# Performance work log

Hardware: AMD Instinct MI355X
Metric: run time of the kernel (lower is better)

## Reference

```python
import jax, jax.numpy as jnp
import numpy as np

N = 20000      # nodes
E = 320000     # edges per metapath graph
M = 3          # metapaths
IN = 256       # input feat dim
HID = 64       # num_hidden per head
NH = 4         # nhead (layer 1)
OUT = 256      # out_dim
NHO = 1        # nhead_out (layer 2)
SA_H = 128     # semantic attention hidden
NEG_SLOPE = 0.2


def gat_conv(h, W, attn_l, attn_r, src, dst, apply_relu):
    # h: [N, F_in]; W: [F_in, H*D]; attn_l/attn_r: [H, D]
    H, D = attn_l.shape
    feat = (h @ W).reshape(N, H, D)                      # [N, H, D]
    el = jnp.sum(feat * attn_l, axis=-1)                 # [N, H]
    er = jnp.sum(feat * attn_r, axis=-1)                 # [N, H]
    e = jax.nn.leaky_relu(el[src] + er[dst], NEG_SLOPE)  # [E, H]
    # edge softmax grouped by destination node
    emax = jax.ops.segment_max(e, dst, num_segments=N)   # [N, H] (-inf for empty)
    emax = jnp.where(jnp.isfinite(emax), emax, 0.0)
    ee = jnp.exp(e - emax[dst])                          # [E, H]
    denom = jax.ops.segment_sum(ee, dst, num_segments=N) # [N, H]
    alpha = ee / (denom[dst] + 1e-9)                     # [E, H]
    msg = alpha[:, :, None] * feat[src]                  # [E, H, D]
    out = jax.ops.segment_sum(msg, dst, num_segments=N)  # [N, H, D]
    out = out.reshape(N, H * D)                          # concat heads
    return jax.nn.relu(out) if apply_relu else out


def semantic_attention(z, W1, b1, v):
    # z: [N, M, F]
    w = jnp.tanh(z @ W1 + b1) @ v          # [N, M, 1]
    w = w.mean(axis=0)                     # [M, 1]
    beta = jax.nn.softmax(w, axis=0)       # [M, 1]
    out = jnp.sum(beta[None, :, :] * z, axis=1)  # [N, F]
    att_mp = beta.squeeze()                # [M]
    return out, att_mp


def setup_inputs() -> dict:
    key = jax.random.key(0)
    ks = jax.random.split(key, 16)
    s = 0.05
    return {
        "x": jax.random.normal(ks[0], (N, IN), dtype=jnp.float32),
        "edges": jax.random.randint(ks[1], (M, 2, E), 0, N, dtype=jnp.int64)
                 if jax.config.jax_enable_x64 else
                 jax.random.randint(ks[1], (M, 2, E), 0, N, dtype=jnp.int32),
        "W1": jax.random.normal(ks[2], (IN, NH * HID), dtype=jnp.float32) * s,
        "al1": jax.random.normal(ks[3], (NH, HID), dtype=jnp.float32) * s,
        "ar1": jax.random.normal(ks[4], (NH, HID), dtype=jnp.float32) * s,
        "saW1": jax.random.normal(ks[5], (NH * HID, SA_H), dtype=jnp.float32) * s,
        "sab1": jnp.zeros((SA_H,), dtype=jnp.float32),
        "sav1": jax.random.normal(ks[6], (SA_H, 1), dtype=jnp.float32) * s,
        "W2": jax.random.normal(ks[7], (NH * HID, NHO * OUT), dtype=jnp.float32) * s,
        "al2": jax.random.normal(ks[8], (NHO, OUT), dtype=jnp.float32) * s,
        "ar2": jax.random.normal(ks[9], (NHO, OUT), dtype=jnp.float32) * s,
        "saW2": jax.random.normal(ks[10], (NHO * OUT, SA_H), dtype=jnp.float32) * s,
        "sab2": jnp.zeros((SA_H,), dtype=jnp.float32),
        "sav2": jax.random.normal(ks[11], (SA_H, 1), dtype=jnp.float32) * s,
    }


def reference(x, edges, W1, al1, ar1, saW1, sab1, sav1,
              W2, al2, ar2, saW2, sab2, sav2):
    h = x
    # HAN layer 1: shared GATConv over each metapath graph, relu activation
    z = jnp.stack([gat_conv(h, W1, al1, ar1, edges[i, 0], edges[i, 1], True)
                   for i in range(M)], axis=1)          # [N, M, NH*HID]
    h, att_mp = semantic_attention(z, saW1, sab1, sav1)
    # HAN layer 2: last layer, no activation (encoding=False)
    z = jnp.stack([gat_conv(h, W2, al2, ar2, edges[i, 0], edges[i, 1], False)
                   for i in range(M)], axis=1)          # [N, M, NHO*OUT]
    h, att_mp = semantic_attention(z, saW2, sab2, sav2)
    return h, att_mp
```

## Files before the change

kernel.cpp:

```cpp
#include <hip/hip_runtime.h>
#include <hip/hip_bf16.h>
#include <math.h>

#define NN 20000
#define EE 320000
#define MM 3
#define FW 256
#define SAH 128
#define NB 79
#define RNG 2500

typedef __attribute__((ext_vector_type(8))) short bf16x8;
typedef __attribute__((ext_vector_type(4))) float f32x4;
typedef __attribute__((ext_vector_type(2))) float f32x2;

static __device__ __forceinline__ float lrelu(float x){ return x > 0.f ? x : 0.2f*x; }

static __device__ __forceinline__ unsigned short f2bf(float f) {
    unsigned u = __float_as_uint(f);
    return (unsigned short)((u + 0x7FFFu + ((u >> 16) & 1u)) >> 16);
}
static __device__ __forceinline__ float bf2f(unsigned short b) {
    return __uint_as_float(((unsigned)b) << 16);
}
static __device__ __forceinline__ float bflo(unsigned u){ return __uint_as_float(u << 16); }
static __device__ __forceinline__ float bfhi(unsigned u){ return __uint_as_float(u & 0xffff0000u); }
static __device__ __forceinline__ unsigned pk2bf(float lo, float hi) {
    return ((unsigned)f2bf(lo)) | (((unsigned)f2bf(hi)) << 16);
}

#define XBLK 2500
#define ZBLK 235
__global__ __launch_bounds__(256) void prep_kernel(const float* __restrict__ x, unsigned short* __restrict__ xb,
                                                   const float* __restrict__ W1, unsigned short* __restrict__ W1t,
                                                   const float* __restrict__ saW1, unsigned short* __restrict__ saW1t,
                                                   const float* __restrict__ W2, unsigned short* __restrict__ W2t,
                                                   const float* __restrict__ saW2, unsigned short* __restrict__ saW2t,
                                                   int* __restrict__ cnt, float* __restrict__ wsum) {
    int b = blockIdx.x, tid = threadIdx.x;
    if (b < XBLK) {
        int i = b*256 + tid;
        const float4* p = (const float4*)x + (size_t)i*2;
        float4 v0 = p[0], v1 = p[1];
        uint4 o;
        o.x = pk2bf(v0.x, v0.y); o.y = pk2bf(v0.z, v0.w);
        o.z = pk2bf(v1.x, v1.y); o.w = pk2bf(v1.z, v1.w);
        ((uint4*)xb)[i] = o;
        return;
    }
    int b2 = b - XBLK;
    if (b2 < 256)      { int n = b2;       W1t  [(size_t)n*256 + tid] = f2bf(W1  [(size_t)tid*256 + n]); return; }
    else if (b2 < 384) { int n = b2 - 256; saW1t[(size_t)n*256 + tid] = f2bf(saW1[(size_t)tid*SAH + n]); return; }
    else if (b2 < 640) { int n = b2 - 384; W2t  [(size_t)n*256 + tid] = f2bf(W2  [(size_t)tid*256 + n]); return; }
    else if (b2 < 768) { int n = b2 - 640; saW2t[(size_t)n*256 + tid] = f2bf(saW2[(size_t)tid*SAH + n]); return; }
    int zb = b2 - 768;
    int i = zb*256 + tid;
    if (i < MM*NN) cnt[i] = 0;
    if (zb == 0 && tid < 8) wsum[tid] = 0.f;
}

__global__ __launch_bounds__(256) void hist_kernel(const int* __restrict__ edges, int* __restrict__ cnt) {
    int m = blockIdx.y;
    int r = blockIdx.x & 7;
    int chunk = blockIdx.x >> 3;
    int e4 = chunk*256 + threadIdx.x;
    if (e4 >= EE/4) return;
    int lo = r * RNG, hi = lo + RNG;
    int4 d = ((const int4*)(edges + (size_t)(m*2+1)*EE))[e4];
    if (d.x >= lo && d.x < hi) atomicAdd(&cnt[m*NN + d.x], 1);
    if (d.y >= lo && d.y < hi) atomicAdd(&cnt[m*NN + d.y], 1);
    if (d.z >= lo && d.z < hi) atomicAdd(&cnt[m*NN + d.z], 1);
    if (d.w >= lo && d.w < hi) atomicAdd(&cnt[m*NN + d.w], 1);
}

__global__ __launch_bounds__(256) void scanA_kernel(const int* __restrict__ cnt, int* __restrict__ rowptr, int* __restrict__ bsum) {
    int m = blockIdx.y;
    int i = blockIdx.x*256 + threadIdx.x;
    int v = (i < NN) ? cnt[m*NN + i] : 0;
    int lane = threadIdx.x & 63;
    int val = v;
    #pragma unroll
    for (int o = 1; o < 64; o <<= 1) { int t = __shfl_up(val, o); if (lane >= o) val += t; }
    __shared__ int ws[4];
    int w = threadIdx.x >> 6;
    if (lane == 63) ws[w] = val;
    __syncthreads();
    #pragma unroll
    for (int j = 0; j < 3; ++j) if (j < w) val += ws[j];
    if (i < NN) rowptr[m*(NN+1) + 1 + i] = val;
    if (threadIdx.x == 255) bsum[m*NB + blockIdx.x] = val;
}

__global__ __launch_bounds__(128) void scanB_kernel(const int* __restrict__ bsum, int* __restrict__ boff) {
    __shared__ int s[128];
    int t = threadIdx.x;
    for (int m = 0; m < MM; ++m) {
        int v = (t < NB) ? bsum[m*NB + t] : 0;
        s[t] = v; __syncthreads();
        for (int o = 1; o < 128; o <<= 1) {
            int x = (t >= o) ? s[t - o] : 0;
            __syncthreads();
            s[t] += x;
            __syncthreads();
        }
        if (t < NB) boff[m*NB + t] = s[t] - v;
        __syncthreads();
    }
}

__global__ __launch_bounds__(256) void scanC_kernel(const int* __restrict__ cnt, int* __restrict__ rowptr,
                                                    const int* __restrict__ boff, int* __restrict__ cursor) {
    int m = blockIdx.y;
    int i = blockIdx.x*256 + threadIdx.x;
    if (i >= NN) return;
    int incl = rowptr[m*(NN+1) + 1 + i] + boff[m*NB + blockIdx.x];
    rowptr[m*(NN+1) + 1 + i] = incl;
    cursor[m*NN + i] = incl - cnt[m*NN + i];
    if (i == 0 && blockIdx.x == 0) rowptr[m*(NN+1)] = 0;
}

__global__ __launch_bounds__(256) void scatter_kernel(const int* __restrict__ edges, int* __restrict__ cursor,
                                                      uint2* __restrict__ csr) {
    int m = blockIdx.y;
    int r = blockIdx.x & 7;
    int chunk = blockIdx.x >> 3;
    int e4 = chunk*256 + threadIdx.x;
    if (e4 >= EE/4) return;
    int lo = r * RNG, hi = lo + RNG;
    int4 s = ((const int4*)(edges + (size_t)(m*2  )*EE))[e4];
    int4 d = ((const int4*)(edges + (size_t)(m*2+1)*EE))[e4];
    if (d.x >= lo && d.x < hi) { int p = atomicAdd(&cursor[m*NN + d.x], 1); csr[(size_t)m*EE + p] = make_uint2((unsigned)s.x, (unsigned)d.x); }
    if (d.y >= lo && d.y < hi) { int p = atomicAdd(&cursor[m*NN + d.y], 1); csr[(size_t)m*EE + p] = make_uint2((unsigned)s.y, (unsigned)d.y); }
    if (d.z >= lo && d.z < hi) { int p = atomicAdd(&cursor[m*NN + d.z], 1); csr[(size_t)m*EE + p] = make_uint2((unsigned)s.z, (unsigned)d.z); }
    if (d.w >= lo && d.w < hi) { int p = atomicAdd(&cursor[m*NN + d.w], 1); csr[(size_t)m*EE + p] = make_uint2((unsigned)s.w, (unsigned)d.w); }
}

template<int H>
__global__ __launch_bounds__(256) void gemm_mfma_kernel(const unsigned short* __restrict__ A,
                                                        const unsigned short* __restrict__ Bt,
                                                        const float* __restrict__ attl, const float* __restrict__ attr,
                                                        unsigned short* __restrict__ C,
                                                        float* __restrict__ el, float* __restrict__ er) {
    int tid = threadIdx.x;
    int w = tid >> 6, lane = tid & 63;
    int rowgrp = w & 1, half = w >> 1;
    int r0 = blockIdx.x*32 + rowgrp*16;
    int colbase = half * 128;
    int lrow = lane & 15, lk = lane >> 4;

    bf16x8 a[8];
    const unsigned short* ap = A + (size_t)(r0 + lrow)*256 + lk*8;
    #pragma unroll
    for (int k = 0; k < 8; ++k) a[k] = *(const bf16x8*)(ap + k*32);

    float pelv[2][4] = {{0.f,0.f,0.f,0.f},{0.f,0.f,0.f,0.f}};
    float perv[2][4] = {{0.f,0.f,0.f,0.f},{0.f,0.f,0.f,0.f}};

    #pragma unroll
    for (int n = 0; n < 8; ++n) {
        int col0 = colbase + n*16;
        const unsigned short* bp = Bt + (size_t)(col0 + lrow)*256 + lk*8;
        f32x4 acc = {0.f, 0.f, 0.f, 0.f};
        #pragma unroll
        for (int k = 0; k < 8; ++k) {
            bf16x8 bfr = *(const bf16x8*)(bp + k*32);
            acc = __builtin_amdgcn_mfma_f32_16x16x32_bf16(a[k], bfr, acc, 0, 0, 0);
        }
        int col = col0 + lrow;
        float al = attl[col], ar = attr[col];
        int hl = (H == 4) ? (n >> 2) : 0;
        #pragma unroll
        for (int r = 0; r < 4; ++r) {
            float cv = acc[r];
            pelv[hl][r] += cv * al;
            perv[hl][r] += cv * ar;
            C[(size_t)(r0 + lk*4 + r)*256 + col] = f2bf(cv);
        }
    }

    int nhl = (H == 4) ? 2 : 1;
    #pragma unroll
    for (int hl = 0; hl < 2; ++hl) {
        if (hl >= nhl) break;
        #pragma unroll
        for (int r = 0; r < 4; ++r) {
            float pe = pelv[hl][r], pr = perv[hl][r];
            #pragma unroll
            for (int o = 1; o < 16; o <<= 1) { pe += __shfl_xor(pe, o); pr += __shfl_xor(pr, o); }
            pelv[hl][r] = pe; perv[hl][r] = pr;
        }
    }

    if (H == 4) {
        if (lrow == 0) {
            int row = r0 + lk*4;
            #pragma unroll
            for (int hl = 0; hl < 2; ++hl) {
                int head = half*2 + hl;
                #pragma unroll
                for (int r = 0; r < 4; ++r) {
                    el[(size_t)(row + r)*4 + head] = pelv[hl][r];
                    er[(size_t)(row + r)*4 + head] = perv[hl][r];
                }
            }
        }
    } else {
        __shared__ float elds[2][32], erds[2][32];
        if (lrow == 0) {
            int rib = rowgrp*16 + lk*4;
            #pragma unroll
            for (int r = 0; r < 4; ++r) {
                elds[half][rib + r] = pelv[0][r];
                erds[half][rib + r] = perv[0][r];
            }
        }
        __syncthreads();
        if (tid < 32) {
            el[blockIdx.x*32 + tid] = elds[0][tid] + elds[1][tid];
            er[blockIdx.x*32 + tid] = erds[0][tid] + erds[1][tid];
        }
    }
}

template<int H>
__global__ __launch_bounds__(256) void edge_ee_kernel(const unsigned long long* __restrict__ csr_ull,
                                                      const float* __restrict__ el, const float* __restrict__ er,
                                                      unsigned short* __restrict__ ee16) {
    int idx = blockIdx.x*256 + threadIdx.x;
    if (idx >= MM*EE/2) return;
    unsigned long long p0 = csr_ull[(size_t)idx*2];
    unsigned long long p1 = csr_ull[(size_t)idx*2 + 1];
    unsigned s0 = (unsigned)p0, d0 = (unsigned)(p0 >> 32);
    unsigned s1 = (unsigned)p1, d1 = (unsigned)(p1 >> 32);
    if (H == 4) {
        float4 l0 = *(const float4*)&el[s0*4];
        float4 r0 = *(const float4*)&er[d0*4];
        float4 l1 = *(const float4*)&el[s1*4];
        float4 r1 = *(const float4*)&er[d1*4];
        uint4 o;
        o.x = pk2bf(expf(lrelu(l0.x + r0.x)), expf(lrelu(l0.y + r0.y)));
        o.y = pk2bf(expf(lrelu(l0.z + r0.z)), expf(lrelu(l0.w + r0.w)));
        o.z = pk2bf(expf(lrelu(l1.x + r1.x)), expf(lrelu(l1.y + r1.y)));
        o.w = pk2bf(expf(lrelu(l1.z + r1.z)), expf(lrelu(l1.w + r1.w)));
        *(uint4*)&ee16[(size_t)idx*8] = o;
    } else {
        unsigned o = pk2bf(expf(lrelu(el[s0] + er[d0])), expf(lrelu(el[s1] + er[d1])));
        *(unsigned*)&ee16[(size_t)idx*2] = o;
    }
}

template<int H, bool RELU>
__global__ __launch_bounds__(256) void agg_kernel(const unsigned short* __restrict__ feat,
                                                  const unsigned short* __restrict__ ee16,
                                                  const int* __restrict__ rowptr,
                                                  const unsigned* __restrict__ csr_u,
                                                  unsigned short* __restrict__ z) {
    int m = blockIdx.y;
    int tid = threadIdx.x;
    int lane = tid & 63, wv = tid >> 6;
    int n = blockIdx.x * 4 + wv;
    int eslot = lane >> 5, flane = lane & 31;
    int h = (H == 4) ? (flane >> 3) : 0;
    int beg = rowptr[m*(NN+1) + n], end = rowptr[m*(NN+1) + n + 1];
    const size_t eb = (size_t)m*EE;

    f32x2 a2[4] = {{0.f,0.f},{0.f,0.f},{0.f,0.f},{0.f,0.f}};
    float den = 0.f;

    int e = beg + eslot;
    unsigned sA = 0, sB = 0;
    float wA = 0.f, wB = 0.f;
    if (e     < end) { sA = csr_u[(eb+e  )*2]; wA = (H==4)? bf2f(ee16[(eb+e  )*4+h]) : bf2f(ee16[eb+e  ]); }
    if (e + 2 < end) { sB = csr_u[(eb+e+2)*2]; wB = (H==4)? bf2f(ee16[(eb+e+2)*4+h]) : bf2f(ee16[eb+e+2]); }

    while (e < end) {
        uint4 v0 = *(const uint4*)(feat + (size_t)sA*256 + flane*8);
        bool h1 = (e + 2 < end);
        uint4 v1 = make_uint4(0,0,0,0);
        if (h1) v1 = *(const uint4*)(feat + (size_t)sB*256 + flane*8);
        float w0 = wA, w1 = h1 ? wB : 0.f;
        if (e + 4 < end) { sA = csr_u[(eb+e+4)*2]; wA = (H==4)? bf2f(ee16[(eb+e+4)*4+h]) : bf2f(ee16[eb+e+4]); }
        if (e + 6 < end) { sB = csr_u[(eb+e+6)*2]; wB = (H==4)? bf2f(ee16[(eb+e+6)*4+h]) : bf2f(ee16[eb+e+6]); }
        den += w0 + w1;
        f32x2 f;
        f.x = bflo(v0.x); f.y = bfhi(v0.x); a2[0] += w0 * f;
        f.x = bflo(v0.y); f.y = bfhi(v0.y); a2[1] += w0 * f;
        f.x = bflo(v0.z); f.y = bfhi(v0.z); a2[2] += w0 * f;
        f.x = bflo(v0.w); f.y = bfhi(v0.w); a2[3] += w0 * f;
        f.x = bflo(v1.x); f.y = bfhi(v1.x); a2[0] += w1 * f;
        f.x = bflo(v1.y); f.y = bfhi(v1.y); a2[1] += w1 * f;
        f.x = bflo(v1.z); f.y = bfhi(v1.z); a2[2] += w1 * f;
        f.x = bflo(v1.w); f.y = bfhi(v1.w); a2[3] += w1 * f;
        e += 4;
    }

    #pragma unroll
    for (int j = 0; j < 4; ++j) {
        a2[j].x += __shfl_xor(a2[j].x, 32);
        a2[j].y += __shfl_xor(a2[j].y, 32);
    }
    den += __shfl_xor(den, 32);

    if (eslot == 0) {
        float inv = 1.f / (den + 1e-9f);
        #pragma unroll
        for (int j = 0; j < 4; ++j) {
            a2[j] *= inv;
            if (RELU) { a2[j].x = fmaxf(a2[j].x, 0.f); a2[j].y = fmaxf(a2[j].y, 0.f); }
        }
        uint4 pk;
        pk.x = pk2bf(a2[0].x, a2[0].y);
        pk.y = pk2bf(a2[1].x, a2[1].y);
        pk.z = pk2bf(a2[2].x, a2[2].y);
        pk.w = pk2bf(a2[3].x, a2[3].y);
        *(uint4*)&z[((size_t)n*MM + m)*256 + flane*8] = pk;
    }
}

__global__ __launch_bounds__(256) void semw_mfma_kernel(const unsigned short* __restrict__ Z,
                                                        const unsigned short* __restrict__ Wt,
                                                        const float* __restrict__ bias, const float* __restrict__ v,
                                                        float* __restrict__ wsum) {
    int tid = threadIdx.x;
    int w = tid >> 6, lane = tid & 63;
    int r0 = blockIdx.x*64 + w*16;
    int lrow = lane & 15, lk = lane >> 4;

    int arow = r0 + lrow;
    if (arow >= NN*MM) arow = NN*MM - 1;
    bf16x8 a[8];
    const unsigned short* ap = Z + (size_t)arow*256 + lk*8;
    #pragma unroll
    for (int k = 0; k < 8; ++k) a[k] = *(const bf16x8*)(ap + k*32);

    float p[4] = {0.f, 0.f, 0.f, 0.f};
    #pragma unroll
    for (int n = 0; n < 8; ++n) {
        int col = n*16 + lrow;
        const unsigned short* bp = Wt + (size_t)col*256 + lk*8;
        f32x4 acc = {0.f, 0.f, 0.f, 0.f};
        #pragma unroll
        for (int k = 0; k < 8; ++k) {
            bf16x8 bfr = *(const bf16x8*)(bp + k*32);
            acc = __builtin_amdgcn_mfma_f32_16x16x32_bf16(a[k], bfr, acc, 0, 0, 0);
        }
        float bb = bias[col], vv = v[col];
        #pragma unroll
        for (int r = 0; r < 4; ++r)
            p[r] += tanhf(acc[r] + bb) * vv;
    }

    #pragma unroll
    for (int r = 0; r < 4; ++r) {
        #pragma unroll
        for (int o = 1; o < 16; o <<= 1) p[r] += __shfl_xor(p[r], o);
    }

    __shared__ float loc[3];
    if (tid < 3) loc[tid] = 0.f;
    __syncthreads();
    if (lrow == 0) {
        #pragma unroll
        for (int r = 0; r < 4; ++r) {
            int row = r0 + lk*4 + r;
            if (row < NN*MM) atomicAdd(&loc[row % MM], p[r]);
        }
    }
    __syncthreads();
    if (tid < 3) atomicAdd(&wsum[tid], loc[tid]);
}

__global__ __launch_bounds__(128) void combine_bf16_kernel(const unsigned short* __restrict__ z, const float* __restrict__ wsum,
                                                           unsigned short* __restrict__ outb) {
    __shared__ float bs[3];
    int n = blockIdx.x, t = threadIdx.x;
    if (t == 0) {
        float w0 = wsum[0] / (float)NN, w1 = wsum[1] / (float)NN, w2 = wsum[2] / (float)NN;
        float mx = fmaxf(w0, fmaxf(w1, w2));
        float e0 = expf(w0 - mx), e1 = expf(w1 - mx), e2 = expf(w2 - mx);
        float s = e0 + e1 + e2;
        bs[0] = e0 / s; bs[1] = e1 / s; bs[2] = e2 / s;
    }
    __syncthreads();
    float b0 = bs[0], b1 = bs[1], b2 = bs[2];
    size_t base = (size_t)n*MM*256 + t*2;
    unsigned z0 = *(const unsigned*)&z[base];
    unsigned z1 = *(const unsigned*)&z[base + 256];
    unsigned z2 = *(const unsigned*)&z[base + 512];
    float ox = b0*bflo(z0) + b1*bflo(z1) + b2*bflo(z2);
    float oy = b0*bfhi(z0) + b1*bfhi(z1) + b2*bfhi(z2);
    *(unsigned*)&outb[(size_t)n*256 + t*2] = pk2bf(ox, oy);
}

__global__ __launch_bounds__(128) void combine_kernel(const unsigned short* __restrict__ z, const float* __restrict__ wsum,
                                                      float* __restrict__ out, float* __restrict__ att_out) {
    __shared__ float bs[3];
    int n = blockIdx.x, t = threadIdx.x;
    if (t == 0) {
        float w0 = wsum[0] / (float)NN, w1 = wsum[1] / (float)NN, w2 = wsum[2] / (float)NN;
        float mx = fmaxf(w0, fmaxf(w1, w2));
        float e0 = expf(w0 - mx), e1 = expf(w1 - mx), e2 = expf(w2 - mx);
        float s = e0 + e1 + e2;
        bs[0] = e0 / s; bs[1] = e1 / s; bs[2] = e2 / s;
        if (n == 0) { att_out[0] = bs[0]; att_out[1] = bs[1]; att_out[2] = bs[2]; }
    }
    __syncthreads();
    float b0 = bs[0], b1 = bs[1], b2 = bs[2];
    size_t base = (size_t)n*MM*256 + t*2;
    unsigned z0 = *(const unsigned*)&z[base];
    unsigned z1 = *(const unsigned*)&z[base + 256];
    unsigned z2 = *(const unsigned*)&z[base + 512];
    float2 o;
    o.x = b0*bflo(z0) + b1*bflo(z1) + b2*bflo(z2);
    o.y = b0*bfhi(z0) + b1*bfhi(z1) + b2*bfhi(z2);
    *(float2*)&out[(size_t)n*256 + t*2] = o;
}

extern "C" void kernel_launch(void* const* d_in, const int* in_sizes, int n_in,
                              void* d_out, int out_size, void* d_ws, size_t ws_size,
                              hipStream_t stream) {
    const float* x    = (const float*)d_in[0];
    const int*   edges= (const int*)  d_in[1];
    const float* W1   = (const float*)d_in[2];
    const float* al1  = (const float*)d_in[3];
    const float* ar1  = (const float*)d_in[4];
    const float* saW1 = (const float*)d_in[5];
    const float* sab1 = (const float*)d_in[6];
    const float* sav1 = (const float*)d_in[7];
    const float* W2   = (const float*)d_in[8];
    const float* al2  = (const float*)d_in[9];
    const float* ar2  = (const float*)d_in[10];
    const float* saW2 = (const float*)d_in[11];
    const float* sab2 = (const float*)d_in[12];
    const float* sav2 = (const float*)d_in[13];
    float* out = (float*)d_out;

    char* ws = (char*)d_ws;
    size_t off = 0;
    auto alloc = [&](size_t bytes) { void* p = ws + off; off += (bytes + 255) & ~(size_t)255; return p; };
    unsigned short* feat  = (unsigned short*)alloc((size_t)NN*256*2);
    unsigned short* z     = (unsigned short*)alloc((size_t)NN*MM*256*2);
    unsigned short* xb    = (unsigned short*)alloc((size_t)NN*256*2);
    unsigned short* W1t   = (unsigned short*)alloc(256*256*2);
    unsigned short* saW1t = (unsigned short*)alloc(SAH*256*2);
    unsigned short* W2t   = (unsigned short*)alloc(256*256*2);
    unsigned short* saW2t = (unsigned short*)alloc(SAH*256*2);
    unsigned short* ee16  = (unsigned short*)alloc((size_t)MM*EE*4*2);
    float* el     = (float*)alloc(NN*4*4);
    float* er     = (float*)alloc(NN*4*4);
    float* wsum   = (float*)alloc(256);
    int*   cnt    = (int*)alloc(MM*NN*4);
    int*   cursor = (int*)alloc(MM*NN*4);
    int*   rowptr = (int*)alloc(MM*(NN+1)*4);
    uint2* csr    = (uint2*)alloc((size_t)MM*EE*8);
    int*   bsum   = (int*)alloc(MM*NB*4);
    int*   boff   = (int*)alloc(MM*NB*4);
    unsigned short* hb = xb;

    int egrid2 = (MM*EE/2 + 255)/256;
    int chunks = (EE/4 + 255)/256;
    dim3 sg(NB, MM);

    prep_kernel<<<XBLK + 768 + ZBLK, 256, 0, stream>>>(x, xb, W1, W1t, saW1, saW1t, W2, W2t, saW2, saW2t, cnt, wsum);

    hist_kernel<<<dim3(chunks*8, MM), 256, 0, stream>>>(edges, cnt);
    scanA_kernel<<<sg, 256, 0, stream>>>(cnt, rowptr, bsum);
    scanB_kernel<<<1, 128, 0, stream>>>(bsum, boff);
    scanC_kernel<<<sg, 256, 0, stream>>>(cnt, rowptr, boff, cursor);
    scatter_kernel<<<dim3(chunks*8, MM), 256, 0, stream>>>(edges, cursor, csr);

    gemm_mfma_kernel<4><<<NN/32, 256, 0, stream>>>(xb, W1t, al1, ar1, feat, el, er);
    edge_ee_kernel<4><<<egrid2, 256, 0, stream>>>((const unsigned long long*)csr, el, er, ee16);
    agg_kernel<4, true><<<dim3(NN/4, MM), 256, 0, stream>>>(feat, ee16, rowptr, (const unsigned*)csr, z);
    semw_mfma_kernel<<<(NN*MM + 63)/64, 256, 0, stream>>>(z, saW1t, sab1, sav1, wsum);
    combine_bf16_kernel<<<NN, 128, 0, stream>>>(z, wsum, hb);

    gemm_mfma_kernel<1><<<NN/32, 256, 0, stream>>>(hb, W2t, al2, ar2, feat, el, er);
    edge_ee_kernel<1><<<egrid2, 256, 0, stream>>>((const unsigned long long*)csr, el, er, ee16);
    agg_kernel<1, false><<<dim3(NN/4, MM), 256, 0, stream>>>(feat, ee16, rowptr, (const unsigned*)csr, z);
    semw_mfma_kernel<<<(NN*MM + 63)/64, 256, 0, stream>>>(z, saW2t, sab2, sav2, wsum + 4);
    combine_kernel<<<NN, 128, 0, stream>>>(z, wsum + 4, out, out + (size_t)NN*256);
}
```

Baseline: 396.8 us.

## Fuse bf16 conversion and semantic combine into GEMM; compact CSR to source-only

The fp32-to-bf16 conversion of x moves out of the prep kernel and into the first GEMM's A-operand load. The layer-1 semantic combine (beta softmax plus weighted sum over metapaths) moves into the second GEMM's A load, which removes a kernel and an intermediate buffer round-trip. The CSR now stores only source indices (4 bytes instead of 8), and edge_ee is rewritten to walk destination rows, loading er once per node. The histogram drops its destination-range partitioning in favour of a flat grid, trading the range filtering for more contended atomics.

Result: no change. 392.3 us (-1.1%).

```diff
diff --git a/kernel.cpp b/kernel.cpp
--- a/kernel.cpp
+++ b/kernel.cpp
@@ -28,27 +28,17 @@
 static __device__ __forceinline__ unsigned pk2bf(float lo, float hi) {
     return ((unsigned)f2bf(lo)) | (((unsigned)f2bf(hi)) << 16);
 }
-
-#define XBLK 2500
+static __device__ __forceinline__ bf16x8 u4_to_bf(uint4 u) {
+    union { uint4 u; bf16x8 b; } c; c.u = u; return c.b;
+}
+
 #define ZBLK 235
-__global__ __launch_bounds__(256) void prep_kernel(const float* __restrict__ x, unsigned short* __restrict__ xb,
-                                                   const float* __restrict__ W1, unsigned short* __restrict__ W1t,
+__global__ __launch_bounds__(256) void prep_kernel(const float* __restrict__ W1, unsigned short* __restrict__ W1t,
                                                    const float* __restrict__ saW1, unsigned short* __restrict__ saW1t,
                                                    const float* __restrict__ W2, unsigned short* __restrict__ W2t,
                                                    const float* __restrict__ saW2, unsigned short* __restrict__ saW2t,
                                                    int* __restrict__ cnt, float* __restrict__ wsum) {
-    int b = blockIdx.x, tid = threadIdx.x;
-    if (b < XBLK) {
-        int i = b*256 + tid;
-        const float4* p = (const float4*)x + (size_t)i*2;
-        float4 v0 = p[0], v1 = p[1];
-        uint4 o;
-        o.x = pk2bf(v0.x, v0.y); o.y = pk2bf(v0.z, v0.w);
-        o.z = pk2bf(v1.x, v1.y); o.w = pk2bf(v1.z, v1.w);
-        ((uint4*)xb)[i] = o;
-        return;
-    }
-    int b2 = b - XBLK;
+    int b2 = blockIdx.x, tid = threadIdx.x;
     if (b2 < 256)      { int n = b2;       W1t  [(size_t)n*256 + tid] = f2bf(W1  [(size_t)tid*256 + n]); return; }
     else if (b2 < 384) { int n = b2 - 256; saW1t[(size_t)n*256 + tid] = f2bf(saW1[(size_t)tid*SAH + n]); return; }
     else if (b2 < 640) { int n = b2 - 384; W2t  [(size_t)n*256 + tid] = f2bf(W2  [(size_t)tid*256 + n]); return; }
@@ -60,17 +50,14 @@
 }
 
 __global__ __launch_bounds__(256) void hist_kernel(const int* __restrict__ edges, int* __restrict__ cnt) {
-    int m = blockIdx.y;
-    int r = blockIdx.x & 7;
-    int chunk = blockIdx.x >> 3;
-    int e4 = chunk*256 + threadIdx.x;
-    if (e4 >= EE/4) return;
-    int lo = r * RNG, hi = lo + RNG;
+    int idx = blockIdx.x*256 + threadIdx.x;
+    if (idx >= MM*EE/4) return;
+    int m = idx / (EE/4), e4 = idx - m*(EE/4);
     int4 d = ((const int4*)(edges + (size_t)(m*2+1)*EE))[e4];
-    if (d.x >= lo && d.x < hi) atomicAdd(&cnt[m*NN + d.x], 1);
-    if (d.y >= lo && d.y < hi) atomicAdd(&cnt[m*NN + d.y], 1);
-    if (d.z >= lo && d.z < hi) atomicAdd(&cnt[m*NN + d.z], 1);
-    if (d.w >= lo && d.w < hi) atomicAdd(&cnt[m*NN + d.w], 1);
+    atomicAdd(&cnt[m*NN + d.x], 1);
+    atomicAdd(&cnt[m*NN + d.y], 1);
+    atomicAdd(&cnt[m*NN + d.z], 1);
+    atomicAdd(&cnt[m*NN + d.w], 1);
 }
 
 __global__ __launch_bounds__(256) void scanA_kernel(const int* __restrict__ cnt, int* __restrict__ rowptr, int* __restrict__ bsum) {
@@ -120,7 +107,7 @@
 }
 
 __global__ __launch_bounds__(256) void scatter_kernel(const int* __restrict__ edges, int* __restrict__ cursor,
-                                                      uint2* __restrict__ csr) {
+                                                      int* __restrict__ csr_src) {
     int m = blockIdx.y;
     int r = blockIdx.x & 7;
     int chunk = blockIdx.x >> 3;
@@ -129,14 +116,16 @@
     int lo = r * RNG, hi = lo + RNG;
     int4 s = ((const int4*)(edges + (size_t)(m*2  )*EE))[e4];
     int4 d = ((const int4*)(edges + (size_t)(m*2+1)*EE))[e4];
-    if (d.x >= lo && d.x < hi) { int p = atomicAdd(&cursor[m*NN + d.x], 1); csr[(size_t)m*EE + p] = make_uint2((unsigned)s.x, (unsigned)d.x); }
-    if (d.y >= lo && d.y < hi) { int p = atomicAdd(&cursor[m*NN + d.y], 1); csr[(size_t)m*EE + p] = make_uint2((unsigned)s.y, (unsigned)d.y); }
-    if (d.z >= lo && d.z < hi) { int p = atomicAdd(&cursor[m*NN + d.z], 1); csr[(size_t)m*EE + p] = make_uint2((unsigned)s.z, (unsigned)d.z); }
-    if (d.w >= lo && d.w < hi) { int p = atomicAdd(&cursor[m*NN + d.w], 1); csr[(size_t)m*EE + p] = make_uint2((unsigned)s.w, (unsigned)d.w); }
-}
-
-template<int H>
-__global__ __launch_bounds__(256) void gemm_mfma_kernel(const unsigned short* __restrict__ A,
+    if (d.x >= lo && d.x < hi) { int p = atomicAdd(&cursor[m*NN + d.x], 1); csr_src[(size_t)m*EE + p] = s.x; }
+    if (d.y >= lo && d.y < hi) { int p = atomicAdd(&cursor[m*NN + d.y], 1); csr_src[(size_t)m*EE + p] = s.y; }
+    if (d.z >= lo && d.z < hi) { int p = atomicAdd(&cursor[m*NN + d.z], 1); csr_src[(size_t)m*EE + p] = s.z; }
+    if (d.w >= lo && d.w < hi) { int p = atomicAdd(&cursor[m*NN + d.w], 1); csr_src[(size_t)m*EE + p] = s.w; }
+}
+
+template<int H, int SRC>
+__global__ __launch_bounds__(256) void gemm_mfma_kernel(const float* __restrict__ Xsrc,
+                                                        const unsigned short* __restrict__ Zsrc,
+                                                        const float* __restrict__ wsum,
                                                         const unsigned short* __restrict__ Bt,
                                                         const float* __restrict__ attl, const float* __restrict__ attr,
                                                         unsigned short* __restrict__ C,
@@ -148,10 +137,46 @@
     int colbase = half * 128;
     int lrow = lane & 15, lk = lane >> 4;
 
+    __shared__ float bsh[3];
+    if (SRC == 2) {
+        if (tid == 0) {
+            float w0 = wsum[0] / (float)NN, w1 = wsum[1] / (float)NN, w2 = wsum[2] / (float)NN;
+            float mx = fmaxf(w0, fmaxf(w1, w2));
+            float e0 = expf(w0 - mx), e1 = expf(w1 - mx), e2 = expf(w2 - mx);
+            float s = e0 + e1 + e2;
+            bsh[0] = e0 / s; bsh[1] = e1 / s; bsh[2] = e2 / s;
+        }
+        __syncthreads();
+    }
+
     bf16x8 a[8];
-    const unsigned short* ap = A + (size_t)(r0 + lrow)*256 + lk*8;
-    #pragma unroll
-    for (int k = 0; k < 8; ++k) a[k] = *(const bf16x8*)(ap + k*32);
+    if (SRC == 0) {
+        const float* xp = Xsrc + (size_t)(r0 + lrow)*256 + lk*8;
+        #pragma unroll
+        for (int k = 0; k < 8; ++k) {
+            float4 v0 = *(const float4*)(xp + k*32);
+            float4 v1 = *(const float4*)(xp + k*32 + 4);
+            uint4 o;
+            o.x = pk2bf(v0.x, v0.y); o.y = pk2bf(v0.z, v0.w);
+            o.z = pk2bf(v1.x, v1.y); o.w = pk2bf(v1.z, v1.w);
+            a[k] = u4_to_bf(o);
+        }
+    } else {
+        float b0 = bsh[0], b1 = bsh[1], b2 = bsh[2];
+        const unsigned short* zp = Zsrc + (size_t)(r0 + lrow)*MM*256 + lk*8;
+        #pragma unroll
+        for (int k = 0; k < 8; ++k) {
+            uint4 z0 = *(const uint4*)(zp + k*32);
+            uint4 z1 = *(const uint4*)(zp + 256 + k*32);
+            uint4 z2 = *(const uint4*)(zp + 512 + k*32);
+            uint4 o;
+            o.x = pk2bf(b0*bflo(z0.x)+b1*bflo(z1.x)+b2*bflo(z2.x), b0*bfhi(z0.x)+b1*bfhi(z1.x)+b2*bfhi(z2.x));
+            o.y = pk2bf(b0*bflo(z0.y)+b1*bflo(z1.y)+b2*bflo(z2.y), b0*bfhi(z0.y)+b1*bfhi(z1.y)+b2*bfhi(z2.y));
+            o.z = pk2bf(b0*bflo(z0.z)+b1*bflo(z1.z)+b2*bflo(z2.z), b0*bfhi(z0.z)+b1*bfhi(z1.z)+b2*bfhi(z2.z));
+            o.w = pk2bf(b0*bflo(z0.w)+b1*bflo(z1.w)+b2*bflo(z2.w), b0*bfhi(z0.w)+b1*bfhi(z1.w)+b2*bfhi(z2.w));
+            a[k] = u4_to_bf(o);
+        }
+    }
 
     float pelv[2][4] = {{0.f,0.f,0.f,0.f},{0.f,0.f,0.f,0.f}};
     float perv[2][4] = {{0.f,0.f,0.f,0.f},{0.f,0.f,0.f,0.f}};
@@ -223,29 +248,32 @@
 }
 
 template<int H>
-__global__ __launch_bounds__(256) void edge_ee_kernel(const unsigned long long* __restrict__ csr_ull,
+__global__ __launch_bounds__(256) void edge_ee_kernel(const int* __restrict__ csr_src,
+                                                      const int* __restrict__ rowptr,
                                                       const float* __restrict__ el, const float* __restrict__ er,
                                                       unsigned short* __restrict__ ee16) {
-    int idx = blockIdx.x*256 + threadIdx.x;
-    if (idx >= MM*EE/2) return;
-    unsigned long long p0 = csr_ull[(size_t)idx*2];
-    unsigned long long p1 = csr_ull[(size_t)idx*2 + 1];
-    unsigned s0 = (unsigned)p0, d0 = (unsigned)(p0 >> 32);
-    unsigned s1 = (unsigned)p1, d1 = (unsigned)(p1 >> 32);
+    int m = blockIdx.y;
+    int tid = threadIdx.x;
+    int g = tid >> 4, gl = tid & 15;
+    int n = blockIdx.x*16 + g;
+    int beg = rowptr[m*(NN+1) + n], end = rowptr[m*(NN+1) + n + 1];
+    const size_t eb = (size_t)m*EE;
     if (H == 4) {
-        float4 l0 = *(const float4*)&el[s0*4];
-        float4 r0 = *(const float4*)&er[d0*4];
-        float4 l1 = *(const float4*)&el[s1*4];
-        float4 r1 = *(const float4*)&er[d1*4];
-        uint4 o;
-        o.x = pk2bf(expf(lrelu(l0.x + r0.x)), expf(lrelu(l0.y + r0.y)));
-        o.y = pk2bf(expf(lrelu(l0.z + r0.z)), expf(lrelu(l0.w + r0.w)));
-        o.z = pk2bf(expf(lrelu(l1.x + r1.x)), expf(lrelu(l1.y + r1.y)));
-        o.w = pk2bf(expf(lrelu(l1.z + r1.z)), expf(lrelu(l1.w + r1.w)));
-        *(uint4*)&ee16[(size_t)idx*8] = o;
+        float4 r4 = *(const float4*)&er[n*4];
+        for (int e = beg + gl; e < end; e += 16) {
+            int src = csr_src[eb + e];
+            float4 l = *(const float4*)&el[src*4];
+            uint2 o;
+            o.x = pk2bf(expf(lrelu(l.x + r4.x)), expf(lrelu(l.y + r4.y)));
+            o.y = pk2bf(expf(lrelu(l.z + r4.z)), expf(lrelu(l.w + r4.w)));
+            *(uint2*)&ee16[(eb + e)*4] = o;
+        }
     } else {
-        unsigned o = pk2bf(expf(lrelu(el[s0] + er[d0])), expf(lrelu(el[s1] + er[d1])));
-        *(unsigned*)&ee16[(size_t)idx*2] = o;
+        float rn = er[n];
+        for (int e = beg + gl; e < end; e += 16) {
+            int src = csr_src[eb + e];
+            ee16[eb + e] = f2bf(expf(lrelu(el[src] + rn)));
+        }
     }
 }
 
@@ -270,8 +298,8 @@
     int e = beg + eslot;
     unsigned sA = 0, sB = 0;
     float wA = 0.f, wB = 0.f;
-    if (e     < end) { sA = csr_u[(eb+e  )*2]; wA = (H==4)? bf2f(ee16[(eb+e  )*4+h]) : bf2f(ee16[eb+e  ]); }
-    if (e + 2 < end) { sB = csr_u[(eb+e+2)*2]; wB = (H==4)? bf2f(ee16[(eb+e+2)*4+h]) : bf2f(ee16[eb+e+2]); }
+    if (e     < end) { sA = csr_u[eb+e  ]; wA = (H==4)? bf2f(ee16[(eb+e  )*4+h]) : bf2f(ee16[eb+e  ]); }
+    if (e + 2 < end) { sB = csr_u[eb+e+2]; wB = (H==4)? bf2f(ee16[(eb+e+2)*4+h]) : bf2f(ee16[eb+e+2]); }
 
     while (e < end) {
         uint4 v0 = *(const uint4*)(feat + (size_t)sA*256 + flane*8);
@@ -279,8 +307,8 @@
         uint4 v1 = make_uint4(0,0,0,0);
         if (h1) v1 = *(const uint4*)(feat + (size_t)sB*256 + flane*8);
         float w0 = wA, w1 = h1 ? wB : 0.f;
-        if (e + 4 < end) { sA = csr_u[(eb+e+4)*2]; wA = (H==4)? bf2f(ee16[(eb+e+4)*4+h]) : bf2f(ee16[eb+e+4]); }
-        if (e + 6 < end) { sB = csr_u[(eb+e+6)*2]; wB = (H==4)? bf2f(ee16[(eb+e+6)*4+h]) : bf2f(ee16[eb+e+6]); }
+        if (e + 4 < end) { sA = csr_u[eb+e+4]; wA = (H==4)? bf2f(ee16[(eb+e+4)*4+h]) : bf2f(ee16[eb+e+4]); }
+        if (e + 6 < end) { sB = csr_u[eb+e+6]; wB = (H==4)? bf2f(ee16[(eb+e+6)*4+h]) : bf2f(ee16[eb+e+6]); }
         den += w0 + w1;
         f32x2 f;
         f.x = bflo(v0.x); f.y = bfhi(v0.x); a2[0] += w0 * f;
@@ -368,28 +396,6 @@
     }
     __syncthreads();
     if (tid < 3) atomicAdd(&wsum[tid], loc[tid]);
-}
-
-__global__ __launch_bounds__(128) void combine_bf16_kernel(const unsigned short* __restrict__ z, const float* __restrict__ wsum,
-                                                           unsigned short* __restrict__ outb) {
-    __shared__ float bs[3];
-    int n = blockIdx.x, t = threadIdx.x;
-    if (t == 0) {
-        float w0 = wsum[0] / (float)NN, w1 = wsum[1] / (float)NN, w2 = wsum[2] / (float)NN;
-        float mx = fmaxf(w0, fmaxf(w1, w2));
-        float e0 = expf(w0 - mx), e1 = expf(w1 - mx), e2 = expf(w2 - mx);
-        float s = e0 + e1 + e2;
-        bs[0] = e0 / s; bs[1] = e1 / s; bs[2] = e2 / s;
-    }
-    __syncthreads();
-    float b0 = bs[0], b1 = bs[1], b2 = bs[2];
-    size_t base = (size_t)n*MM*256 + t*2;
-    unsigned z0 = *(const unsigned*)&z[base];
-    unsigned z1 = *(const unsigned*)&z[base + 256];
-    unsigned z2 = *(const unsigned*)&z[base + 512];
-    float ox = b0*bflo(z0) + b1*bflo(z1) + b2*bflo(z2);
-    float oy = b0*bfhi(z0) + b1*bfhi(z1) + b2*bfhi(z2);
-    *(unsigned*)&outb[(size_t)n*256 + t*2] = pk2bf(ox, oy);
 }
 
 __global__ __launch_bounds__(128) void combine_kernel(const unsigned short* __restrict__ z, const float* __restrict__ wsum,
@@ -440,7 +446,6 @@
     auto alloc = [&](size_t bytes) { void* p = ws + off; off += (bytes + 255) & ~(size_t)255; return p; };
     unsigned short* feat  = (unsigned short*)alloc((size_t)NN*256*2);
     unsigned short* z     = (unsigned short*)alloc((size_t)NN*MM*256*2);
-    unsigned short* xb    = (unsigned short*)alloc((size_t)NN*256*2);
     unsigned short* W1t   = (unsigned short*)alloc(256*256*2);
     unsigned short* saW1t = (unsigned short*)alloc(SAH*256*2);
     unsigned short* W2t   = (unsigned short*)alloc(256*256*2);
@@ -452,32 +457,30 @@
     int*   cnt    = (int*)alloc(MM*NN*4);
     int*   cursor = (int*)alloc(MM*NN*4);
     int*   rowptr = (int*)alloc(MM*(NN+1)*4);
-    uint2* csr    = (uint2*)alloc((size_t)MM*EE*8);
+    int*   csr_s  = (int*)alloc((size_t)MM*EE*4);
     int*   bsum   = (int*)alloc(MM*NB*4);
     int*   boff   = (int*)alloc(MM*NB*4);
-    unsigned short* hb = xb;
-
-    int egrid2 = (MM*EE/2 + 255)/256;
+
+    int egrid4 = (MM*EE/4 + 255)/256;
     int chunks = (EE/4 + 255)/256;
     dim3 sg(NB, MM);
 
-    prep_kernel<<<XBLK + 768 + ZBLK, 256, 0, stream>>>(x, xb, W1, W1t, saW1, saW1t, W2, W2t, saW2, saW2t, cnt, wsum);
-
-    hist_kernel<<<dim3(chunks*8, MM), 256, 0, stream>>>(edges, cnt);
+    prep_kernel<<<768 + ZBLK, 256, 0, stream>>>(W1, W1t, saW1, saW1t, W2, W2t, saW2, saW2t, cnt, wsum);
+
+    hist_kernel<<<egrid4, 256, 0, stream>>>(edges, cnt);
     scanA_kernel<<<sg, 256, 0, stream>>>(cnt, rowptr, bsum);
     scanB_kernel<<<1, 128, 0, stream>>>(bsum, boff);
     scanC_kernel<<<sg, 256, 0, stream>>>(cnt, rowptr, boff, cursor);
-    scatter_kernel<<<dim3(chunks*8, MM), 256, 0, stream>>>(edges, cursor, csr);
-
-    gemm_mfma_kernel<4><<<NN/32, 256, 0, stream>>>(xb, W1t, al1, ar1, feat, el, er);
-    edge_ee_kernel<4><<<egrid2, 256, 0, stream>>>((const unsigned long long*)csr, el, er, ee16);
-    agg_kernel<4, true><<<dim3(NN/4, MM), 256, 0, stream>>>(feat, ee16, rowptr, (const unsigned*)csr, z);
+    scatter_kernel<<<dim3(chunks*8, MM), 256, 0, stream>>>(edges, cursor, csr_s);
+
+    gemm_mfma_kernel<4, 0><<<NN/32, 256, 0, stream>>>(x, nullptr, nullptr, W1t, al1, ar1, feat, el, er);
+    edge_ee_kernel<4><<<dim3(NN/16, MM), 256, 0, stream>>>(csr_s, rowptr, el, er, ee16);
+    agg_kernel<4, true><<<dim3(NN/4, MM), 256, 0, stream>>>(feat, ee16, rowptr, (const unsigned*)csr_s, z);
     semw_mfma_kernel<<<(NN*MM + 63)/64, 256, 0, stream>>>(z, saW1t, sab1, sav1, wsum);
-    combine_bf16_kernel<<<NN, 128, 0, stream>>>(z, wsum, hb);
-
-    gemm_mfma_kernel<1><<<NN/32, 256, 0, stream>>>(hb, W2t, al2, ar2, feat, el, er);
-    edge_ee_kernel<1><<<egrid2, 256, 0, stream>>>((const unsigned long long*)csr, el, er, ee16);
-    agg_kernel<1, false><<<dim3(NN/4, MM), 256, 0, stream>>>(feat, ee16, rowptr, (const unsigned*)csr, z);
+
+    gemm_mfma_kernel<1, 2><<<NN/32, 256, 0, stream>>>(nullptr, z, wsum, W2t, al2, ar2, feat, el, er);
+    edge_ee_kernel<1><<<dim3(NN/16, MM), 256, 0, stream>>>(csr_s, rowptr, el, er, ee16);
+    agg_kernel<1, false><<<dim3(NN/4, MM), 256, 0, stream>>>(feat, ee16, rowptr, (const unsigned*)csr_s, z);
     semw_mfma_kernel<<<(NN*MM + 63)/64, 256, 0, stream>>>(z, saW2t, sab2, sav2, wsum + 4);
     combine_kernel<<<NN, 128, 0, stream>>>(z, wsum + 4, out, out + (size_t)NN*256);
 }
```
